# Optimization experiments

Hardware: AMD Instinct MI355X
Metric: run time of the kernel (lower is better)

## Reference

```python
import jax, jax.numpy as jnp
import numpy as np

BASIS_ORDER = 7  # basis_dim = 8 (Chebyshev T_0..T_7 of tanh(x))


def chebyshev_basis(x, order=BASIS_ORDER):
    """x: [batch, in] -> [batch, in, order+1] Chebyshev basis on tanh(x)."""
    xt = jnp.tanh(x)
    terms = [jnp.ones_like(xt), xt]
    for _ in range(2, order + 1):
        terms.append(2.0 * xt * terms[-1] - terms[-2])
    return jnp.stack(terms[: order + 1], axis=-1)


def setup_inputs() -> dict:
    key = jax.random.key(0)
    k1, k2, k3 = jax.random.split(key, 3)
    batch, in_f, out_f, K = 4096, 1024, 1024, BASIS_ORDER + 1
    x = jax.random.normal(k1, (batch, in_f), dtype=jnp.float32)
    # Kaiming-uniform-ish init scale
    bound = 1.0 / np.sqrt(in_f * K)
    weights = jax.random.uniform(k2, (out_f, in_f, K), dtype=jnp.float32,
                                 minval=-bound, maxval=bound)
    bias_param = jax.random.uniform(k3, (out_f,), dtype=jnp.float32,
                                    minval=-bound, maxval=bound)
    return {"x": x, "weights": weights, "bias_param": bias_param}


def reference(x, weights, bias_param):
    # basis: [b, i, k]; weights: [o, i, k] -> out[b, o] = sum_{i,k} basis*W
    basis = chebyshev_basis(x)  # [batch, in, K]
    out = jnp.einsum('bik,oik->bo', basis, weights)
    return out + bias_param
```

## Files before the change

### kernel.cpp

```cpp
#include <hip/hip_runtime.h>
#include <hip/hip_bf16.h>

#define MD 4096
#define ND 1024
#define KD 8192
#define IN_F 1024

typedef __bf16 bf16x8 __attribute__((ext_vector_type(8)));
typedef float f32x4 __attribute__((ext_vector_type(4)));

#define N_BASIS (MD * IN_F)
#define N_CONV ((ND * KD) / 8)

__global__ __launch_bounds__(256) void prep_kernel(
    const float* __restrict__ x, const float* __restrict__ w,
    __bf16* __restrict__ A, __bf16* __restrict__ B) {
  int i = blockIdx.x * blockDim.x + threadIdx.x;
  if (i < N_BASIS) {
    float t = tanhf(x[i]);
    float two_t = 2.0f * t;
    float T0 = 1.0f;
    float T1 = t;
    float T2 = two_t * T1 - T0;
    float T3 = two_t * T2 - T1;
    float T4 = two_t * T3 - T2;
    float T5 = two_t * T4 - T3;
    float T6 = two_t * T5 - T4;
    float T7 = two_t * T6 - T5;
    bf16x8 v;
    v[0] = (__bf16)T0; v[1] = (__bf16)T1; v[2] = (__bf16)T2; v[3] = (__bf16)T3;
    v[4] = (__bf16)T4; v[5] = (__bf16)T5; v[6] = (__bf16)T6; v[7] = (__bf16)T7;
    *(bf16x8*)(A + (size_t)i * 8) = v;
  } else if (i < N_BASIS + N_CONV) {
    int j = i - N_BASIS;
    const float4* p = (const float4*)(w + (size_t)j * 8);
    float4 a = p[0], b = p[1];
    bf16x8 v;
    v[0] = (__bf16)a.x; v[1] = (__bf16)a.y; v[2] = (__bf16)a.z; v[3] = (__bf16)a.w;
    v[4] = (__bf16)b.x; v[5] = (__bf16)b.y; v[6] = (__bf16)b.z; v[7] = (__bf16)b.w;
    *(bf16x8*)(B + (size_t)j * 8) = v;
  }
}

#define BM 64
#define BN 128
#define BK 64

__global__ __launch_bounds__(256) void gemm_bias(
    const __bf16* __restrict__ A, const __bf16* __restrict__ B,
    const float* __restrict__ bias, float* __restrict__ C) {
  __shared__ __align__(16) __bf16 As[BM * BK];
  __shared__ __align__(16) __bf16 Bs[BN * BK];

  const int tid = threadIdx.x;
  const int wave = tid >> 6;
  const int lane = tid & 63;
  const int n0 = blockIdx.x * BN;
  const int m0 = blockIdx.y * BM;
  const int wm = wave >> 1;
  const int wn = wave & 1;

  const int ar = lane >> 3;
  const int swz_col = ((lane & 7) ^ ar) * 8;
  const __bf16* gA = A + (size_t)(m0 + wave * 16 + ar) * KD + swz_col;
  const __bf16* gB = B + (size_t)(n0 + wave * 32 + ar) * KD + swz_col;
  const __bf16* lA = As + (wave * 16) * BK;
  const __bf16* lB = Bs + (wave * 32) * BK;

  f32x4 acc[2][4];
#pragma unroll
  for (int i = 0; i < 2; i++)
#pragma unroll
    for (int j = 0; j < 4; j++) acc[i][j] = (f32x4){0.f, 0.f, 0.f, 0.f};

  const int fr = lane & 15;
  const int fr7 = fr & 7;
  const int qk = lane >> 4;

  for (int kt = 0; kt < KD; kt += BK) {
#pragma unroll
    for (int j = 0; j < 2; j++)
      __builtin_amdgcn_global_load_lds(
          (const __attribute__((address_space(1))) void*)(gA + kt + (size_t)j * 8 * KD),
          (__attribute__((address_space(3))) void*)(lA + j * 8 * BK), 16, 0, 0);
#pragma unroll
    for (int j = 0; j < 4; j++)
      __builtin_amdgcn_global_load_lds(
          (const __attribute__((address_space(1))) void*)(gB + kt + (size_t)j * 8 * KD),
          (__attribute__((address_space(3))) void*)(lB + j * 8 * BK), 16, 0, 0);
    __syncthreads();

#pragma unroll
    for (int s = 0; s < 2; s++) {
      const int pa = ((s * 4 + qk) ^ fr7) * 8;
      bf16x8 af[2], bfr[4];
#pragma unroll
      for (int mi = 0; mi < 2; mi++)
        af[mi] = *(const bf16x8*)&As[(wm * 32 + mi * 16 + fr) * BK + pa];
#pragma unroll
      for (int ni = 0; ni < 4; ni++)
        bfr[ni] = *(const bf16x8*)&Bs[(wn * 64 + ni * 16 + fr) * BK + pa];
#pragma unroll
      for (int mi = 0; mi < 2; mi++)
#pragma unroll
        for (int ni = 0; ni < 4; ni++)
          acc[mi][ni] = __builtin_amdgcn_mfma_f32_16x16x32_bf16(
              af[mi], bfr[ni], acc[mi][ni], 0, 0, 0);
    }
    __syncthreads();
  }

  const int col0 = n0 + wn * 64;
  const int row0 = m0 + wm * 32 + (lane >> 4) * 4;
#pragma unroll
  for (int ni = 0; ni < 4; ni++) {
    int col = col0 + ni * 16 + (lane & 15);
    float bv = bias[col];
#pragma unroll
    for (int mi = 0; mi < 2; mi++) {
      int row = row0 + mi * 16;
#pragma unroll
      for (int r = 0; r < 4; r++)
        C[(size_t)(row + r) * ND + col] = acc[mi][ni][r] + bv;
    }
  }
}

extern "C" void kernel_launch(void* const* d_in, const int* in_sizes, int n_in,
                              void* d_out, int out_size, void* d_ws, size_t ws_size,
                              hipStream_t stream) {
  const float* x = (const float*)d_in[0];
  const float* w = (const float*)d_in[1];
  const float* bias = (const float*)d_in[2];
  float* out = (float*)d_out;

  __bf16* Abf = (__bf16*)d_ws;
  __bf16* Bbf = (__bf16*)((char*)d_ws + (size_t)MD * KD * 2);

  {
    int n = N_BASIS + N_CONV;
    prep_kernel<<<(n + 255) / 256, 256, 0, stream>>>(x, w, Abf, Bbf);
  }
  {
    dim3 grid(ND / BN, MD / BM);
    gemm_bias<<<grid, 256, 0, stream>>>(Abf, Bbf, bias, out);
  }
}
```

Before: 200.3 us.

## Pre-swizzle operands into MFMA fragment layout and run LDS-free register GEMM

The prep kernel now writes A and B in a tiled layout matching the 16x16x32 MFMA fragment order, so each lane loads its fragment straight from global memory with one 16-byte load. The GEMM drops shared memory and barriers entirely, uses a 128x128 block tile with a 4x4 MFMA tile per wave, and double-buffers fragments in registers. This removes LDS traffic and syncs, but every wave now reads its A/B fragments independently from global/L2 with no intra-block sharing through LDS, and the prefetch depth is only one k-block.

```diff
diff --git a/kernel.cpp b/kernel.cpp
--- a/kernel.cpp
+++ b/kernel.cpp
@@ -5,35 +5,49 @@
 #define ND 1024
 #define KD 8192
 #define IN_F 1024
+#define KBLKS (KD / 32)
+#define MT (MD / 16)
+#define NT (ND / 16)
 
 typedef __bf16 bf16x8 __attribute__((ext_vector_type(8)));
 typedef float f32x4 __attribute__((ext_vector_type(4)));
 
-#define N_BASIS (MD * IN_F)
-#define N_CONV ((ND * KD) / 8)
+#define N_A (MT * KBLKS * 64)
+#define N_B (NT * KBLKS * 64)
 
 __global__ __launch_bounds__(256) void prep_kernel(
     const float* __restrict__ x, const float* __restrict__ w,
     __bf16* __restrict__ A, __bf16* __restrict__ B) {
-  int i = blockIdx.x * blockDim.x + threadIdx.x;
-  if (i < N_BASIS) {
-    float t = tanhf(x[i]);
-    float two_t = 2.0f * t;
+  int t = blockIdx.x * blockDim.x + threadIdx.x;
+  if (t < N_A) {
+    int L = t & 63;
+    int kb = (t >> 6) & (KBLKS - 1);
+    int mt = t >> 14;
+    int b = mt * 16 + (L & 15);
+    int i = kb * 4 + (L >> 4);
+    float v = x[(size_t)b * IN_F + i];
+    float tt = tanhf(v);
+    float two_t = 2.0f * tt;
     float T0 = 1.0f;
-    float T1 = t;
+    float T1 = tt;
     float T2 = two_t * T1 - T0;
     float T3 = two_t * T2 - T1;
     float T4 = two_t * T3 - T2;
     float T5 = two_t * T4 - T3;
     float T6 = two_t * T5 - T4;
     float T7 = two_t * T6 - T5;
-    bf16x8 v;
-    v[0] = (__bf16)T0; v[1] = (__bf16)T1; v[2] = (__bf16)T2; v[3] = (__bf16)T3;
-    v[4] = (__bf16)T4; v[5] = (__bf16)T5; v[6] = (__bf16)T6; v[7] = (__bf16)T7;
-    *(bf16x8*)(A + (size_t)i * 8) = v;
-  } else if (i < N_BASIS + N_CONV) {
-    int j = i - N_BASIS;
-    const float4* p = (const float4*)(w + (size_t)j * 8);
+    bf16x8 o;
+    o[0] = (__bf16)T0; o[1] = (__bf16)T1; o[2] = (__bf16)T2; o[3] = (__bf16)T3;
+    o[4] = (__bf16)T4; o[5] = (__bf16)T5; o[6] = (__bf16)T6; o[7] = (__bf16)T7;
+    *(bf16x8*)(A + (size_t)t * 8) = o;
+  } else if (t < N_A + N_B) {
+    int j = t - N_A;
+    int L = j & 63;
+    int kb = (j >> 6) & (KBLKS - 1);
+    int nt = j >> 14;
+    int o_ = nt * 16 + (L & 15);
+    int i = kb * 4 + (L >> 4);
+    const float4* p = (const float4*)(w + ((size_t)o_ * IN_F + i) * 8);
     float4 a = p[0], b = p[1];
     bf16x8 v;
     v[0] = (__bf16)a.x; v[1] = (__bf16)a.y; v[2] = (__bf16)a.z; v[3] = (__bf16)a.w;
@@ -42,82 +56,92 @@
   }
 }
 
-#define BM 64
-#define BN 128
-#define BK 64
-
-__global__ __launch_bounds__(256) void gemm_bias(
+__global__ __launch_bounds__(256) void gemm_reg(
     const __bf16* __restrict__ A, const __bf16* __restrict__ B,
     const float* __restrict__ bias, float* __restrict__ C) {
-  __shared__ __align__(16) __bf16 As[BM * BK];
-  __shared__ __align__(16) __bf16 Bs[BN * BK];
-
   const int tid = threadIdx.x;
   const int wave = tid >> 6;
   const int lane = tid & 63;
-  const int n0 = blockIdx.x * BN;
-  const int m0 = blockIdx.y * BM;
   const int wm = wave >> 1;
   const int wn = wave & 1;
+  const int mt0 = blockIdx.y * 8 + wm * 4;
+  const int nt0 = blockIdx.x * 8 + wn * 4;
 
-  const int ar = lane >> 3;
-  const int swz_col = ((lane & 7) ^ ar) * 8;
-  const __bf16* gA = A + (size_t)(m0 + wave * 16 + ar) * KD + swz_col;
-  const __bf16* gB = B + (size_t)(n0 + wave * 32 + ar) * KD + swz_col;
-  const __bf16* lA = As + (wave * 16) * BK;
-  const __bf16* lB = Bs + (wave * 32) * BK;
+  const __bf16* pa[4];
+  const __bf16* pb[4];
+#pragma unroll
+  for (int i = 0; i < 4; i++) {
+    pa[i] = A + (((size_t)(mt0 + i) * KBLKS) * 64 + lane) * 8;
+    pb[i] = B + (((size_t)(nt0 + i) * KBLKS) * 64 + lane) * 8;
+  }
 
-  f32x4 acc[2][4];
+  f32x4 acc[4][4];
 #pragma unroll
-  for (int i = 0; i < 2; i++)
+  for (int i = 0; i < 4; i++)
 #pragma unroll
     for (int j = 0; j < 4; j++) acc[i][j] = (f32x4){0.f, 0.f, 0.f, 0.f};
 
-  const int fr = lane & 15;
-  const int fr7 = fr & 7;
-  const int qk = lane >> 4;
+  bf16x8 a0[4], b0[4], a1[4], b1[4];
+#pragma unroll
+  for (int i = 0; i < 4; i++) {
+    a0[i] = *(const bf16x8*)(pa[i]);
+    b0[i] = *(const bf16x8*)(pb[i]);
+  }
 
-  for (int kt = 0; kt < KD; kt += BK) {
+  for (int kb = 0; kb < KBLKS - 2; kb += 2) {
 #pragma unroll
-    for (int j = 0; j < 2; j++)
-      __builtin_amdgcn_global_load_lds(
-          (const __attribute__((address_space(1))) void*)(gA + kt + (size_t)j * 8 * KD),
-          (__attribute__((address_space(3))) void*)(lA + j * 8 * BK), 16, 0, 0);
+    for (int i = 0; i < 4; i++) {
+      a1[i] = *(const bf16x8*)(pa[i] + (size_t)(kb + 1) * 512);
+      b1[i] = *(const bf16x8*)(pb[i] + (size_t)(kb + 1) * 512);
+    }
 #pragma unroll
-    for (int j = 0; j < 4; j++)
-      __builtin_amdgcn_global_load_lds(
-          (const __attribute__((address_space(1))) void*)(gB + kt + (size_t)j * 8 * KD),
-          (__attribute__((address_space(3))) void*)(lB + j * 8 * BK), 16, 0, 0);
-    __syncthreads();
-
-#pragma unroll
-    for (int s = 0; s < 2; s++) {
-      const int pa = ((s * 4 + qk) ^ fr7) * 8;
-      bf16x8 af[2], bfr[4];
-#pragma unroll
-      for (int mi = 0; mi < 2; mi++)
-        af[mi] = *(const bf16x8*)&As[(wm * 32 + mi * 16 + fr) * BK + pa];
+    for (int mi = 0; mi < 4; mi++)
 #pragma unroll
       for (int ni = 0; ni < 4; ni++)
-        bfr[ni] = *(const bf16x8*)&Bs[(wn * 64 + ni * 16 + fr) * BK + pa];
+        acc[mi][ni] = __builtin_amdgcn_mfma_f32_16x16x32_bf16(
+            a0[mi], b0[ni], acc[mi][ni], 0, 0, 0);
 #pragma unroll
-      for (int mi = 0; mi < 2; mi++)
+    for (int i = 0; i < 4; i++) {
+      a0[i] = *(const bf16x8*)(pa[i] + (size_t)(kb + 2) * 512);
+      b0[i] = *(const bf16x8*)(pb[i] + (size_t)(kb + 2) * 512);
+    }
 #pragma unroll
-        for (int ni = 0; ni < 4; ni++)
-          acc[mi][ni] = __builtin_amdgcn_mfma_f32_16x16x32_bf16(
-              af[mi], bfr[ni], acc[mi][ni], 0, 0, 0);
+    for (int mi = 0; mi < 4; mi++)
+#pragma unroll
+      for (int ni = 0; ni < 4; ni++)
+        acc[mi][ni] = __builtin_amdgcn_mfma_f32_16x16x32_bf16(
+            a1[mi], b1[ni], acc[mi][ni], 0, 0, 0);
+  }
+  {
+    const int kb = KBLKS - 2;
+#pragma unroll
+    for (int i = 0; i < 4; i++) {
+      a1[i] = *(const bf16x8*)(pa[i] + (size_t)(kb + 1) * 512);
+      b1[i] = *(const bf16x8*)(pb[i] + (size_t)(kb + 1) * 512);
     }
-    __syncthreads();
+#pragma unroll
+    for (int mi = 0; mi < 4; mi++)
+#pragma unroll
+      for (int ni = 0; ni < 4; ni++)
+        acc[mi][ni] = __builtin_amdgcn_mfma_f32_16x16x32_bf16(
+            a0[mi], b0[ni], acc[mi][ni], 0, 0, 0);
+#pragma unroll
+    for (int mi = 0; mi < 4; mi++)
+#pragma unroll
+      for (int ni = 0; ni < 4; ni++)
+        acc[mi][ni] = __builtin_amdgcn_mfma_f32_16x16x32_bf16(
+            a1[mi], b1[ni], acc[mi][ni], 0, 0, 0);
   }
 
-  const int col0 = n0 + wn * 64;
-  const int row0 = m0 + wm * 32 + (lane >> 4) * 4;
+  const int m0 = blockIdx.y * 128 + wm * 64;
+  const int n0 = blockIdx.x * 128 + wn * 64;
+  const int row0 = m0 + (lane >> 4) * 4;
 #pragma unroll
   for (int ni = 0; ni < 4; ni++) {
-    int col = col0 + ni * 16 + (lane & 15);
+    int col = n0 + ni * 16 + (lane & 15);
     float bv = bias[col];
 #pragma unroll
-    for (int mi = 0; mi < 2; mi++) {
+    for (int mi = 0; mi < 4; mi++) {
       int row = row0 + mi * 16;
 #pragma unroll
       for (int r = 0; r < 4; r++)
@@ -138,11 +162,11 @@
   __bf16* Bbf = (__bf16*)((char*)d_ws + (size_t)MD * KD * 2);
 
   {
-    int n = N_BASIS + N_CONV;
+    int n = N_A + N_B;
     prep_kernel<<<(n + 255) / 256, 256, 0, stream>>>(x, w, Abf, Bbf);
   }
   {
-    dim3 grid(ND / BN, MD / BM);
-    gemm_bias<<<grid, 256, 0, stream>>>(Abf, Bbf, bias, out);
+    dim3 grid(ND / 128, MD / 128);
+    gemm_reg<<<grid, 256, 0, stream>>>(Abf, Bbf, bias, out);
   }
 }
```

Measured after the change: 248.6 us. 24.1% more time.

## Double-buffer LDS tiles and enlarge GEMM block tile to 128x128

Applied to the files above, without the earlier changes.

Adds a two-stage LDS ping-pong so the global-to-LDS loads for the next K tile are issued before the MFMA work on the current tile, leaving one barrier per iteration. BM grows from 64 to 128, so each wave computes a 64x64 sub-tile (4x4 MFMA accumulators) and gets more reuse of each loaded A and B fragment. The aim is to hide global load latency and cut memory traffic per FLOP. In exchange it uses more LDS (64KB) and more accumulator registers, and the grid halves to 256 blocks, which lowers occupancy and parallelism.

```diff
diff --git a/kernel.cpp b/kernel.cpp
--- a/kernel.cpp
+++ b/kernel.cpp
@@ -42,15 +42,16 @@
   }
 }
 
-#define BM 64
+#define BM 128
 #define BN 128
 #define BK 64
+#define KITERS (KD / BK)
 
 __global__ __launch_bounds__(256) void gemm_bias(
     const __bf16* __restrict__ A, const __bf16* __restrict__ B,
     const float* __restrict__ bias, float* __restrict__ C) {
-  __shared__ __align__(16) __bf16 As[BM * BK];
-  __shared__ __align__(16) __bf16 Bs[BN * BK];
+  __shared__ __align__(16) __bf16 As[2][BM * BK];
+  __shared__ __align__(16) __bf16 Bs[2][BN * BK];
 
   const int tid = threadIdx.x;
   const int wave = tid >> 6;
@@ -62,14 +63,14 @@
 
   const int ar = lane >> 3;
   const int swz_col = ((lane & 7) ^ ar) * 8;
-  const __bf16* gA = A + (size_t)(m0 + wave * 16 + ar) * KD + swz_col;
+  const __bf16* gA = A + (size_t)(m0 + wave * 32 + ar) * KD + swz_col;
   const __bf16* gB = B + (size_t)(n0 + wave * 32 + ar) * KD + swz_col;
-  const __bf16* lA = As + (wave * 16) * BK;
-  const __bf16* lB = Bs + (wave * 32) * BK;
+  const int ldsOffA = (wave * 32) * BK;
+  const int ldsOffB = (wave * 32) * BK;
 
-  f32x4 acc[2][4];
+  f32x4 acc[4][4];
 #pragma unroll
-  for (int i = 0; i < 2; i++)
+  for (int i = 0; i < 4; i++)
 #pragma unroll
     for (int j = 0; j < 4; j++) acc[i][j] = (f32x4){0.f, 0.f, 0.f, 0.f};
 
@@ -77,31 +78,49 @@
   const int fr7 = fr & 7;
   const int qk = lane >> 4;
 
-  for (int kt = 0; kt < KD; kt += BK) {
 #pragma unroll
-    for (int j = 0; j < 2; j++)
-      __builtin_amdgcn_global_load_lds(
-          (const __attribute__((address_space(1))) void*)(gA + kt + (size_t)j * 8 * KD),
-          (__attribute__((address_space(3))) void*)(lA + j * 8 * BK), 16, 0, 0);
+  for (int j = 0; j < 4; j++) {
+    __builtin_amdgcn_global_load_lds(
+        (const __attribute__((address_space(1))) void*)(gA + (size_t)j * 8 * KD),
+        (__attribute__((address_space(3))) void*)(&As[0][ldsOffA + j * 8 * BK]),
+        16, 0, 0);
+    __builtin_amdgcn_global_load_lds(
+        (const __attribute__((address_space(1))) void*)(gB + (size_t)j * 8 * KD),
+        (__attribute__((address_space(3))) void*)(&Bs[0][ldsOffB + j * 8 * BK]),
+        16, 0, 0);
+  }
+  __syncthreads();
+
+#pragma unroll 2
+  for (int kt = 0; kt < KITERS; kt++) {
+    const int cur = kt & 1;
+    const int nxt = cur ^ 1;
+    if (kt + 1 < KITERS) {
+      const int g = (kt + 1) * BK;
 #pragma unroll
-    for (int j = 0; j < 4; j++)
-      __builtin_amdgcn_global_load_lds(
-          (const __attribute__((address_space(1))) void*)(gB + kt + (size_t)j * 8 * KD),
-          (__attribute__((address_space(3))) void*)(lB + j * 8 * BK), 16, 0, 0);
-    __syncthreads();
-
+      for (int j = 0; j < 4; j++) {
+        __builtin_amdgcn_global_load_lds(
+            (const __attribute__((address_space(1))) void*)(gA + g + (size_t)j * 8 * KD),
+            (__attribute__((address_space(3))) void*)(&As[nxt][ldsOffA + j * 8 * BK]),
+            16, 0, 0);
+        __builtin_amdgcn_global_load_lds(
+            (const __attribute__((address_space(1))) void*)(gB + g + (size_t)j * 8 * KD),
+            (__attribute__((address_space(3))) void*)(&Bs[nxt][ldsOffB + j * 8 * BK]),
+            16, 0, 0);
+      }
+    }
 #pragma unroll
     for (int s = 0; s < 2; s++) {
       const int pa = ((s * 4 + qk) ^ fr7) * 8;
-      bf16x8 af[2], bfr[4];
+      bf16x8 af[4], bfr[4];
 #pragma unroll
-      for (int mi = 0; mi < 2; mi++)
-        af[mi] = *(const bf16x8*)&As[(wm * 32 + mi * 16 + fr) * BK + pa];
+      for (int mi = 0; mi < 4; mi++)
+        af[mi] = *(const bf16x8*)&As[cur][(wm * 64 + mi * 16 + fr) * BK + pa];
 #pragma unroll
       for (int ni = 0; ni < 4; ni++)
-        bfr[ni] = *(const bf16x8*)&Bs[(wn * 64 + ni * 16 + fr) * BK + pa];
+        bfr[ni] = *(const bf16x8*)&Bs[cur][(wn * 64 + ni * 16 + fr) * BK + pa];
 #pragma unroll
-      for (int mi = 0; mi < 2; mi++)
+      for (int mi = 0; mi < 4; mi++)
 #pragma unroll
         for (int ni = 0; ni < 4; ni++)
           acc[mi][ni] = __builtin_amdgcn_mfma_f32_16x16x32_bf16(
@@ -110,14 +129,14 @@
     __syncthreads();
   }
 
+  const int row0 = m0 + wm * 64 + (lane >> 4) * 4;
   const int col0 = n0 + wn * 64;
-  const int row0 = m0 + wm * 32 + (lane >> 4) * 4;
 #pragma unroll
   for (int ni = 0; ni < 4; ni++) {
     int col = col0 + ni * 16 + (lane & 15);
     float bv = bias[col];
 #pragma unroll
-    for (int mi = 0; mi < 2; mi++) {
+    for (int mi = 0; mi < 4; mi++) {
       int row = row0 + mi * 16;
 #pragma unroll
       for (int r = 0; r < 4; r++)
```

Result: slower. 240.7 us (+20.2%).
